# Kernel tuning notes

Hardware: AMD Instinct MI355X
Metric: run time of the kernel (lower is better)

Reference implementation:

```python
import jax, jax.numpy as jnp
import numpy as np

DIM = 768
HEADS = 8
HIDDEN = 3072
B, Hs, Ws = 16, 32, 32
N = Hs * Ws
LN_EPS = 1e-5


def setup_inputs() -> dict:
    key = jax.random.key(0)
    ks = jax.random.split(key, 10)
    s = lambda *sh: 0.02
    return {
        "x": jax.random.normal(ks[0], (B, N, DIM), jnp.float32),
        "Wq": jax.random.normal(ks[1], (DIM, DIM), jnp.float32) * 0.02,
        "temperature": jnp.ones((HEADS, 1, 1), jnp.float32),
        "fc1_w": jax.random.normal(ks[2], (HIDDEN, DIM), jnp.float32) * 0.02,
        "fc1_b": jnp.zeros((HIDDEN,), jnp.float32),
        "dw_w": jax.random.normal(ks[3], (HIDDEN, 1, 3, 3), jnp.float32) * 0.1,
        "dw_b": jnp.zeros((HIDDEN,), jnp.float32),
        "gamma": jnp.ones((HIDDEN,), jnp.float32),
        "fc2_w": jax.random.normal(ks[4], (DIM, HIDDEN), jnp.float32) * 0.02,
        "fc2_b": jnp.zeros((DIM,), jnp.float32),
        "ln_w": jnp.ones((DIM,), jnp.float32),
        "ln_b": jnp.zeros((DIM,), jnp.float32),
        "H": Hs,
        "W": Ws,
    }


def _dwconv(x, w, b, H, W):
    # x: (B, N, hidden) -> depthwise 3x3, pad 1 -> (B, N, hidden)
    Bn, Nn, Ch = x.shape
    img = x.transpose(0, 2, 1).reshape(Bn, Ch, H, W)
    out = jax.lax.conv_general_dilated(
        img, w, window_strides=(1, 1), padding=((1, 1), (1, 1)),
        dimension_numbers=("NCHW", "OIHW", "NCHW"), feature_group_count=Ch)
    out = out + b[None, :, None, None]
    return out.reshape(Bn, Ch, Nn).transpose(0, 2, 1)


def _layernorm(x, w, b):
    mu = x.mean(-1, keepdims=True)
    var = ((x - mu) ** 2).mean(-1, keepdims=True)
    return (x - mu) * jax.lax.rsqrt(var + LN_EPS) * w + b


def reference(x, Wq, temperature, fc1_w, fc1_b, dw_w, dw_b, gamma,
              fc2_w, fc2_b, ln_w, ln_b, H, W):
    # gpd_ratio == active_ratio == 1 -> pre/post scalings cancel
    Bn, Nn, C = x.shape
    h = temperature.shape[0]
    Ch = C // h
    # q/k/v heads: (B, h, N, Ch)
    q = (x @ Wq.T).reshape(Bn, Nn, h, Ch).transpose(0, 2, 1, 3)
    kv = x.reshape(Bn, Nn, h, Ch).transpose(0, 2, 1, 3)
    # channel attention: softmax over N, pool k over Ch, sigmoid gate
    qs = jax.nn.softmax(q, axis=-2).transpose(0, 1, 3, 2)      # (B,h,Ch,N)
    kp = jax.nn.softmax(kv, axis=-2).mean(-1, keepdims=True)    # (B,h,N,1)
    attn = jax.nn.sigmoid(qs @ kp) * temperature                # (B,h,Ch,1)
    # MLP on v (== x after scaling cancels): fc1 -> dwconv residual -> fc2 -> LN
    h1 = x @ fc1_w.T + fc1_b                                    # (B,N,hidden)
    h2 = gamma * _dwconv(h1, dw_w, dw_b, H, W) + h1
    v = _layernorm(h2 @ fc2_w.T + fc2_b, ln_w, ln_b)            # (B,N,C)
    v = v.reshape(Bn, Nn, h, Ch).transpose(0, 2, 1, 3)          # (B,h,N,Ch)
    prod = attn * v.transpose(0, 1, 3, 2)                       # (B,h,Ch,N)
    out = prod.transpose(0, 3, 1, 2).reshape(Bn, Nn, C)
    return out, prod.transpose(0, 1, 3, 2)
```

## Files before the change

### kernel.cpp

```cpp
#include <hip/hip_runtime.h>

#define BATCH 16
#define SEQ   1024
#define DIM   768
#define NHEAD 8
#define CHD   96
#define HID   3072
#define MTOT  (BATCH * SEQ)

using u16 = unsigned short;
typedef __attribute__((ext_vector_type(8))) short bf16x8;
typedef __attribute__((ext_vector_type(4))) float f32x4;

#define AS1 __attribute__((address_space(1)))
#define AS3 __attribute__((address_space(3)))

__device__ inline float bf2f(u16 u) {
    union { unsigned int i; float f; } v; v.i = ((unsigned int)u) << 16; return v.f;
}
__device__ inline u16 f2bf(float f) {
    union { float f; unsigned int i; } v; v.f = f;
    unsigned int r = v.i + 0x7FFFu + ((v.i >> 16) & 1u);
    return (u16)(r >> 16);
}

__device__ inline void gld16(const void* g, void* l) {
    __builtin_amdgcn_global_load_lds((AS1 const void*)g, (AS3 void*)l, 16, 0, 0);
}

template <int BM>
__global__ __launch_bounds__(512) void gemm_p(const u16* __restrict__ A,
                                              const u16* __restrict__ B,
                                              const float* __restrict__ bias,
                                              u16* __restrict__ C1, int N1,
                                              u16* __restrict__ C2,
                                              int M, int N, int K) {
    constexpr int AROUNDS = BM / 128;
    constexpr int ASLOT = BM * 32;
    constexpr int AFOLD = BM / 2;
    constexpr int NFI = BM / 32;
    __shared__ u16 lds[4 * (ASLOT + 8192)];

    const int tid = threadIdx.x;
    const int lane = tid & 63;
    const int wid = tid >> 6;
    const int wm = (wid >> 2) * (BM / 2);
    const int wn = (wid & 3) << 6;

    const int nwg = gridDim.x;
    const int wg = blockIdx.x;
    const int lid = (wg & 7) * (nwg >> 3) + (wg >> 3);
    const int nbx = N >> 8;
    const int mb = lid / nbx, nb = lid - mb * nbx;
    const int m0 = mb * BM, n0 = nb << 8;

    const int sprow = tid >> 3;
    const int s_l = (tid & 7) ^ (sprow & 7);
    const int sgk = (s_l & 3) << 3;
    const u16* pa = A + (size_t)(m0 + (s_l >> 2) * AFOLD + sprow) * K + sgk;
    const u16* pb = B + (size_t)(n0 + (s_l >> 2) * 128 + sprow) * K + sgk;
    const size_t r64K = (size_t)64 * K;

#define STAGE_A(slot, k0) do {                                        \
    gld16(pa + (k0), &lds[(slot) * (ASLOT + 8192) + tid * 8]);        \
    if (AROUNDS == 2)                                                 \
        gld16(pa + (k0) + r64K,                                       \
              &lds[(slot) * (ASLOT + 8192) + 4096 + tid * 8]);        \
} while (0)
#define STAGE_B(slot, k0) do {                                        \
    gld16(pb + (k0), &lds[(slot) * (ASLOT + 8192) + ASLOT + tid * 8]);\
    gld16(pb + (k0) + r64K,                                           \
          &lds[(slot) * (ASLOT + 8192) + ASLOT + 4096 + tid * 8]);    \
} while (0)

    const int lrow = lane & 15;
    const int kg = lane >> 4;
    const int xA = (((wid >> 2) * 4 + kg) ^ (lrow & 7)) << 3;
    const int xB = (((wn >> 7) * 4 + kg) ^ (lrow & 7)) << 3;
    const int bbase = (wn & 64) + lrow;

    f32x4 acc[NFI][4] = {};

    const int NT = K >> 5;
    STAGE_A(0, 0);  STAGE_B(0, 0);
    STAGE_A(1, 32); STAGE_B(1, 32);
    STAGE_A(2, 64); STAGE_B(2, 64);

    for (int t = 0; t < NT; ++t) {
        const int rem = NT - 1 - t;
        if (rem >= 2)      asm volatile("s_waitcnt vmcnt(8)" ::: "memory");
        else if (rem == 1) asm volatile("s_waitcnt vmcnt(4)" ::: "memory");
        else               asm volatile("s_waitcnt vmcnt(0)" ::: "memory");
        __builtin_amdgcn_sched_barrier(0);
        __builtin_amdgcn_s_barrier();

        const u16* Ls = &lds[(t & 3) * (ASLOT + 8192)];
        const int k3 = (t + 3) << 5;

        bf16x8 bfr[4], af[NFI / 2];
#pragma unroll
        for (int j = 0; j < 4; ++j)
            bfr[j] = *(const bf16x8*)&Ls[ASLOT + (bbase + j * 16) * 64 + xB];
#pragma unroll
        for (int i = 0; i < NFI / 2; ++i)
            af[i] = *(const bf16x8*)&Ls[(i * 16 + lrow) * 64 + xA];
        if (rem >= 3) STAGE_A((t + 3) & 3, k3);
        asm volatile("s_waitcnt lgkmcnt(0)" ::: "memory");
        __builtin_amdgcn_sched_barrier(0);
        __builtin_amdgcn_s_setprio(1);
#pragma unroll
        for (int i = 0; i < NFI / 2; ++i)
#pragma unroll
            for (int j = 0; j < 4; ++j)
                acc[i][j] = __builtin_amdgcn_mfma_f32_16x16x32_bf16(af[i], bfr[j], acc[i][j], 0, 0, 0);
        __builtin_amdgcn_s_setprio(0);

        bf16x8 af2[NFI / 2];
#pragma unroll
        for (int i = 0; i < NFI / 2; ++i)
            af2[i] = *(const bf16x8*)&Ls[((i + NFI / 2) * 16 + lrow) * 64 + xA];
        if (rem >= 3) STAGE_B((t + 3) & 3, k3);
        asm volatile("s_waitcnt lgkmcnt(0)" ::: "memory");
        __builtin_amdgcn_sched_barrier(0);
        __builtin_amdgcn_s_setprio(1);
#pragma unroll
        for (int i = 0; i < NFI / 2; ++i)
#pragma unroll
            for (int j = 0; j < 4; ++j)
                acc[i + NFI / 2][j] = __builtin_amdgcn_mfma_f32_16x16x32_bf16(af2[i], bfr[j], acc[i + NFI / 2][j], 0, 0, 0);
        __builtin_amdgcn_s_setprio(0);
    }
#undef STAGE_A
#undef STAGE_B

    __builtin_amdgcn_s_barrier();
    u16* Ct = lds;
    const int crow = (lane >> 4) << 2, ccol = lane & 15;
#pragma unroll
    for (int i = 0; i < NFI; ++i) {
#pragma unroll
        for (int j = 0; j < 4; ++j) {
            const int col = wn + j * 16 + ccol;
            const int gn = n0 + col;
            const float bv = (gn < N1) ? bias[gn] : 0.f;
#pragma unroll
            for (int r = 0; r < 4; ++r) {
                const int row = wm + i * 16 + crow + r;
                const int slot = (col >> 3) ^ (row & 7);
                Ct[row * 256 + slot * 8 + (col & 7)] = f2bf(acc[i][j][r] + bv);
            }
        }
    }
    __builtin_amdgcn_s_barrier();
    const int N2 = N - N1;
#pragma unroll
    for (int k = 0; k < BM / 16; ++k) {
        const int c = tid + (k << 9);
        const int row = c >> 5, s = c & 31;
        bf16x8 v = *(const bf16x8*)&Ct[row * 256 + ((s ^ (row & 7)) << 3)];
        const int gm = m0 + row, gnb = n0 + (s << 3);
        if (gnb < N1)
            *(bf16x8*)&C1[(size_t)gm * N1 + gnb] = v;
        else
            *(bf16x8*)&C2[(size_t)gm * N2 + gnb - N1] = v;
    }
}

__global__ __launch_bounds__(256) void cvt_all(const float* __restrict__ x,
                                               const float* __restrict__ Wq,
                                               const float* __restrict__ w1,
                                               const float* __restrict__ w2,
                                               u16* __restrict__ xb,
                                               u16* __restrict__ Wqb,
                                               u16* __restrict__ w1b,
                                               u16* __restrict__ w2b) {
    const int E0 = MTOT * DIM / 4;
    const int E1 = E0 + DIM * DIM / 4;
    const int E2 = E1 + HID * DIM / 4;
    const int E3 = E2 + DIM * HID / 4;
    int i = blockIdx.x * 256 + threadIdx.x;
    if (i >= E3) return;
    const float* in; u16* out; int k;
    if (i < E0)      { in = x;  out = xb;  k = i; }
    else if (i < E1) { in = Wq; out = Wqb; k = i - E0; }
    else if (i < E2) { in = w1; out = w1b; k = i - E1; }
    else             { in = w2; out = w2b; k = i - E2; }
    float4 v = reinterpret_cast<const float4*>(in)[k];
    ushort4 o;
    o.x = f2bf(v.x); o.y = f2bf(v.y); o.z = f2bf(v.z); o.w = f2bf(v.w);
    reinterpret_cast<ushort4*>(out)[k] = o;
}

__global__ __launch_bounds__(256) void colsm_stats(const u16* __restrict__ X,
                                                   float* __restrict__ Mo,
                                                   float* __restrict__ So) {
    const int tid = threadIdx.x, lane = tid & 63, chunk = tid >> 6;
    const int b = blockIdx.y;
    const int j = blockIdx.x * 64 + lane;
    const u16* p = X + (size_t)b * SEQ * DIM + j;
    float m = -3.0e38f, s = 0.f;
    const int nEnd = (chunk + 1) << 8;
    for (int n = chunk << 8; n < nEnd; ++n) {
        float raw = bf2f(p[(size_t)n * DIM]);
        float nm = fmaxf(m, raw);
        s = s * __expf(m - nm) + __expf(raw - nm);
        m = nm;
    }
    __shared__ float ms[4][64], ss[4][64];
    ms[chunk][lane] = m; ss[chunk][lane] = s;
    __syncthreads();
    if (tid < 64) {
        float M = fmaxf(fmaxf(ms[0][lane], ms[1][lane]), fmaxf(ms[2][lane], ms[3][lane]));
        float S = ss[0][lane] * __expf(ms[0][lane] - M) + ss[1][lane] * __expf(ms[1][lane] - M) +
                  ss[2][lane] * __expf(ms[2][lane] - M) + ss[3][lane] * __expf(ms[3][lane] - M);
        Mo[b * DIM + j] = M;
        So[b * DIM + j] = S;
    }
}

__global__ __launch_bounds__(256) void kp_k(const u16* __restrict__ x,
                                            const float* __restrict__ Mx,
                                            const float* __restrict__ Sx,
                                            float* __restrict__ kp) {
    const int n = blockIdx.x, b = blockIdx.y, tid = threadIdx.x;
    const u16* row = x + ((size_t)b * SEQ + n) * DIM;
    const int h = tid >> 5, c0 = tid & 31;
    const float* Mrow = Mx + b * DIM;
    const float* Srow = Sx + b * DIM;
    float s = 0.f;
#pragma unroll
    for (int q = 0; q < 3; ++q) {
        const int j = h * CHD + c0 + (q << 5);
        s += __expf(bf2f(row[j]) - Mrow[j]) / Srow[j];
    }
#pragma unroll
    for (int o = 16; o; o >>= 1) s += __shfl_down(s, o, 32);
    if (c0 == 0) kp[((size_t)b * NHEAD + h) * SEQ + n] = s * (1.f / (float)CHD);
}

__global__ __launch_bounds__(256) void qattn_k(const u16* __restrict__ Q,
                                               const float* __restrict__ kp,
                                               const float* __restrict__ temp,
                                               float* __restrict__ attnv) {
    const int tid = threadIdx.x, lane = tid & 63, chunk = tid >> 6;
    const int b = blockIdx.y;
    const int j = blockIdx.x * 64 + lane;
    const int h = j / CHD;
    const u16* qp = Q + (size_t)b * SEQ * DIM + j;
    const float* kpp = kp + ((size_t)b * NHEAD + h) * SEQ;
    float m = -3.0e38f, s = 0.f, a = 0.f;
    const int nEnd = (chunk + 1) << 8;
    for (int n = chunk << 8; n < nEnd; ++n) {
        float q = bf2f(qp[(size_t)n * DIM]);
        float nm = fmaxf(m, q);
        float sc = __expf(m - nm), e = __expf(q - nm);
        s = s * sc + e;
        a = a * sc + e * kpp[n];
        m = nm;
    }
    __shared__ float ms[4][64], ss[4][64], as_[4][64];
    ms[chunk][lane] = m; ss[chunk][lane] = s; as_[chunk][lane] = a;
    __syncthreads();
    if (tid < 64) {
        float M = fmaxf(fmaxf(ms[0][lane], ms[1][lane]), fmaxf(ms[2][lane], ms[3][lane]));
        float S = 0.f, A = 0.f;
#pragma unroll
        for (int c = 0; c < 4; ++c) {
            float sc = __expf(ms[c][lane] - M);
            S += ss[c][lane] * sc;
            A += as_[c][lane] * sc;
        }
        float z = A / S;
        attnv[b * DIM + j] = temp[h] / (1.f + __expf(-z));
    }
}

__global__ __launch_bounds__(128) void dwconv_v(const u16* __restrict__ h1,
                                                const float* __restrict__ w,
                                                const float* __restrict__ dwb,
                                                const float* __restrict__ gamma,
                                                u16* __restrict__ h2) {
    const int g = blockIdx.x * 128 + threadIdx.x;
    const int y = blockIdx.y >> 2;
    const int xw0 = (blockIdx.y & 3) << 3;
    const int b = blockIdx.z;
    const int ch0 = g << 3;

    float wreg[8][9], bias2[8];
#pragma unroll
    for (int c = 0; c < 8; ++c) {
        const float gm = gamma[ch0 + c];
#pragma unroll
        for (int k = 0; k < 9; ++k) wreg[c][k] = gm * w[(ch0 + c) * 9 + k];
        wreg[c][4] += 1.0f;
        bias2[c] = gm * dwb[ch0 + c];
    }

    float acc[8][8];
#pragma unroll
    for (int xo = 0; xo < 8; ++xo)
#pragma unroll
        for (int c = 0; c < 8; ++c) acc[xo][c] = bias2[c];

    const u16* base = h1 + (size_t)b * SEQ * HID + ch0;
#pragma unroll
    for (int dy = 0; dy < 3; ++dy) {
        const int yy = y + dy - 1;
        if ((unsigned)yy > 31u) continue;
#pragma unroll
        for (int cr = -1; cr <= 8; ++cr) {
            const int col = xw0 + cr;
            if ((unsigned)col > 31u) continue;
            const uint4 v = *reinterpret_cast<const uint4*>(
                base + (size_t)((yy << 5) + col) * HID);
            float f[8];
            f[0] = bf2f((u16)(v.x & 0xffff)); f[1] = bf2f((u16)(v.x >> 16));
            f[2] = bf2f((u16)(v.y & 0xffff)); f[3] = bf2f((u16)(v.y >> 16));
            f[4] = bf2f((u16)(v.z & 0xffff)); f[5] = bf2f((u16)(v.z >> 16));
            f[6] = bf2f((u16)(v.w & 0xffff)); f[7] = bf2f((u16)(v.w >> 16));
            const int xlo = cr > 0 ? cr - 1 : 0;
            const int xhi = cr < 7 ? cr + 1 : 7;
#pragma unroll
            for (int xo = 0; xo < 8; ++xo) {
                if (xo < xlo || xo > xhi) continue;
                const int dx = cr - xo + 1;
#pragma unroll
                for (int c = 0; c < 8; ++c)
                    acc[xo][c] += f[c] * wreg[c][dy * 3 + dx];
            }
        }
    }

#pragma unroll
    for (int xo = 0; xo < 8; ++xo) {
        const int n = (y << 5) + xw0 + xo;
        uint4 o;
        o.x = (unsigned)f2bf(acc[xo][0]) | ((unsigned)f2bf(acc[xo][1]) << 16);
        o.y = (unsigned)f2bf(acc[xo][2]) | ((unsigned)f2bf(acc[xo][3]) << 16);
        o.z = (unsigned)f2bf(acc[xo][4]) | ((unsigned)f2bf(acc[xo][5]) << 16);
        o.w = (unsigned)f2bf(acc[xo][6]) | ((unsigned)f2bf(acc[xo][7]) << 16);
        *reinterpret_cast<uint4*>(h2 + ((size_t)b * SEQ + n) * HID + ch0) = o;
    }
}

__global__ __launch_bounds__(256) void ln_out_k(const u16* __restrict__ vpre,
                                                const float* __restrict__ lnw,
                                                const float* __restrict__ lnb,
                                                const float* __restrict__ attnv,
                                                float* __restrict__ out,
                                                float* __restrict__ out2) {
    const int n = blockIdx.x, b = blockIdx.y, tid = threadIdx.x;
    __shared__ float red[4];
    const u16* row = vpre + ((size_t)b * SEQ + n) * DIM;
    float v[3];
    float s = 0.f;
#pragma unroll
    for (int q = 0; q < 3; ++q) { v[q] = bf2f(row[tid + (q << 8)]); s += v[q]; }
#pragma unroll
    for (int o = 32; o; o >>= 1) s += __shfl_down(s, o, 64);
    if ((tid & 63) == 0) red[tid >> 6] = s;
    __syncthreads();
    const float mu = (red[0] + red[1] + red[2] + red[3]) * (1.f / (float)DIM);
    __syncthreads();
    float vs = 0.f;
#pragma unroll
    for (int q = 0; q < 3; ++q) { float d = v[q] - mu; vs += d * d; }
#pragma unroll
    for (int o = 32; o; o >>= 1) vs += __shfl_down(vs, o, 64);
    if ((tid & 63) == 0) red[tid >> 6] = vs;
    __syncthreads();
    const float rstd = rsqrtf((red[0] + red[1] + red[2] + red[3]) * (1.f / (float)DIM) + 1e-5f);
    const float* at = attnv + b * DIM;
    float* orow = out + ((size_t)b * SEQ + n) * DIM;
#pragma unroll
    for (int q = 0; q < 3; ++q) {
        int j = tid + (q << 8);
        float o = (v[q] - mu) * rstd * lnw[j] + lnb[j];
        o *= at[j];
        orow[j] = o;
        int h = j / CHD, c = j - h * CHD;
        out2[(((size_t)b * NHEAD + h) * SEQ + n) * CHD + c] = o;
    }
}

extern "C" void kernel_launch(void* const* d_in, const int* in_sizes, int n_in,
                              void* d_out, int out_size, void* d_ws, size_t ws_size,
                              hipStream_t stream) {
    const float* x     = (const float*)d_in[0];
    const float* Wq    = (const float*)d_in[1];
    const float* temp  = (const float*)d_in[2];
    const float* fc1w  = (const float*)d_in[3];
    const float* fc1b  = (const float*)d_in[4];
    const float* dww   = (const float*)d_in[5];
    const float* dwb   = (const float*)d_in[6];
    const float* gamma = (const float*)d_in[7];
    const float* fc2w  = (const float*)d_in[8];
    const float* fc2b  = (const float*)d_in[9];
    const float* lnw   = (const float*)d_in[10];
    const float* lnb   = (const float*)d_in[11];

    float* out  = (float*)d_out;
    float* out2 = out + (size_t)BATCH * SEQ * DIM;

    char* ws = (char*)d_ws;
    u16* xb     = (u16*)ws;
    u16* h1     = (u16*)(ws + 25165824);
    u16* Bbig   = (u16*)(ws + 125829120);
    u16* Wqb    = Bbig + (size_t)HID * DIM;
    u16* fc2wb  = (u16*)(ws + 131727360);
    float* Mx   = (float*)(ws + 136445952);
    float* Sx   = Mx + BATCH * DIM;
    float* kp   = Sx + BATCH * DIM;
    float* attnv = kp + BATCH * NHEAD * SEQ;
    u16* vpreb  = xb;

    u16* Qb = (u16*)d_out;
    u16* h2 = (u16*)d_out;

    {
        const int tot4 = (MTOT * DIM + DIM * DIM + HID * DIM + DIM * HID) / 4;
        cvt_all<<<(tot4 + 255) / 256, 256, 0, stream>>>(
            x, Wq, fc1w, fc2w, xb, Wqb, Bbig, fc2wb);
    }

    gemm_p<256><<<(MTOT / 256) * (3840 / 256), 512, 0, stream>>>(
        xb, Bbig, fc1b, h1, HID, Qb, MTOT, HID + DIM, DIM);

    colsm_stats<<<dim3(DIM / 64, BATCH), 256, 0, stream>>>(xb, Mx, Sx);
    kp_k<<<dim3(SEQ, BATCH), 256, 0, stream>>>(xb, Mx, Sx, kp);
    qattn_k<<<dim3(DIM / 64, BATCH), 256, 0, stream>>>(Qb, kp, temp, attnv);

    dwconv_v<<<dim3(3, 128, BATCH), 128, 0, stream>>>(h1, dww, dwb, gamma, h2);
    gemm_p<256><<<(MTOT / 256) * (DIM / 256), 512, 0, stream>>>(
        h2, fc2wb, fc2b, vpreb, DIM, (u16*)nullptr, MTOT, DIM, HID);
    ln_out_k<<<dim3(SEQ, BATCH), 256, 0, stream>>>(vpreb, lnw, lnb, attnv, out, out2);
}
```

Measured before the change: 377.8 us.

## Load B fragments directly from global memory, staging only A through LDS

The GEMM no longer stages the B tile through LDS. Each wave now reads its B fragments straight from global memory into registers every k-step, while A keeps the 4-slot global_load_lds ring. This shrinks LDS use and is meant to raise occupancy and cut LDS traffic, at the cost of uncoalesced direct global reads of B and some exposed latency. To fit the smaller LDS, the epilogue writes the C tile in two halves, and the vmcnt wait counts are retuned for the new number of outstanding loads.

```diff
diff --git a/kernel.cpp b/kernel.cpp
--- a/kernel.cpp
+++ b/kernel.cpp
@@ -39,12 +39,12 @@
     constexpr int ASLOT = BM * 32;
     constexpr int AFOLD = BM / 2;
     constexpr int NFI = BM / 32;
-    __shared__ u16 lds[4 * (ASLOT + 8192)];
+    __shared__ u16 lds[4 * ASLOT];
 
     const int tid = threadIdx.x;
     const int lane = tid & 63;
     const int wid = tid >> 6;
-    const int wm = (wid >> 2) * (BM / 2);
+    const int wm = (wid >> 2) * AFOLD;
     const int wn = (wid & 3) << 6;
 
     const int nwg = gridDim.x;
@@ -58,49 +58,52 @@
     const int s_l = (tid & 7) ^ (sprow & 7);
     const int sgk = (s_l & 3) << 3;
     const u16* pa = A + (size_t)(m0 + (s_l >> 2) * AFOLD + sprow) * K + sgk;
-    const u16* pb = B + (size_t)(n0 + (s_l >> 2) * 128 + sprow) * K + sgk;
     const size_t r64K = (size_t)64 * K;
 
 #define STAGE_A(slot, k0) do {                                        \
-    gld16(pa + (k0), &lds[(slot) * (ASLOT + 8192) + tid * 8]);        \
+    gld16(pa + (k0), &lds[(slot) * ASLOT + tid * 8]);                 \
     if (AROUNDS == 2)                                                 \
-        gld16(pa + (k0) + r64K,                                       \
-              &lds[(slot) * (ASLOT + 8192) + 4096 + tid * 8]);        \
-} while (0)
-#define STAGE_B(slot, k0) do {                                        \
-    gld16(pb + (k0), &lds[(slot) * (ASLOT + 8192) + ASLOT + tid * 8]);\
-    gld16(pb + (k0) + r64K,                                           \
-          &lds[(slot) * (ASLOT + 8192) + ASLOT + 4096 + tid * 8]);    \
+        gld16(pa + (k0) + r64K, &lds[(slot) * ASLOT + 4096 + tid * 8]);\
 } while (0)
 
     const int lrow = lane & 15;
     const int kg = lane >> 4;
     const int xA = (((wid >> 2) * 4 + kg) ^ (lrow & 7)) << 3;
-    const int xB = (((wn >> 7) * 4 + kg) ^ (lrow & 7)) << 3;
-    const int bbase = (wn & 64) + lrow;
+    const u16* Bp = B + (size_t)(n0 + wn + lrow) * K + (kg << 3);
 
     f32x4 acc[NFI][4] = {};
 
     const int NT = K >> 5;
-    STAGE_A(0, 0);  STAGE_B(0, 0);
-    STAGE_A(1, 32); STAGE_B(1, 32);
-    STAGE_A(2, 64); STAGE_B(2, 64);
+    STAGE_A(0, 0);
+    STAGE_A(1, 32);
+    STAGE_A(2, 64);
 
     for (int t = 0; t < NT; ++t) {
         const int rem = NT - 1 - t;
-        if (rem >= 2)      asm volatile("s_waitcnt vmcnt(8)" ::: "memory");
-        else if (rem == 1) asm volatile("s_waitcnt vmcnt(4)" ::: "memory");
-        else               asm volatile("s_waitcnt vmcnt(0)" ::: "memory");
+        if (t >= 2) {
+            if constexpr (AROUNDS == 2) asm volatile("s_waitcnt vmcnt(12)" ::: "memory");
+            else                        asm volatile("s_waitcnt vmcnt(10)" ::: "memory");
+        } else if (t == 1) {
+            if constexpr (AROUNDS == 2) asm volatile("s_waitcnt vmcnt(8)" ::: "memory");
+            else                        asm volatile("s_waitcnt vmcnt(6)" ::: "memory");
+        } else {
+            if constexpr (AROUNDS == 2) asm volatile("s_waitcnt vmcnt(4)" ::: "memory");
+            else                        asm volatile("s_waitcnt vmcnt(2)" ::: "memory");
+        }
         __builtin_amdgcn_sched_barrier(0);
         __builtin_amdgcn_s_barrier();
-
-        const u16* Ls = &lds[(t & 3) * (ASLOT + 8192)];
+        __builtin_amdgcn_sched_barrier(0);
+
+        bf16x8 bfr[4];
+#pragma unroll
+        for (int j = 0; j < 4; ++j)
+            bfr[j] = *(const bf16x8*)(Bp + (size_t)(j * 16) * K + (t << 5));
+        __builtin_amdgcn_sched_barrier(0);
+
+        const u16* Ls = &lds[(t & 3) * ASLOT];
         const int k3 = (t + 3) << 5;
 
-        bf16x8 bfr[4], af[NFI / 2];
-#pragma unroll
-        for (int j = 0; j < 4; ++j)
-            bfr[j] = *(const bf16x8*)&Ls[ASLOT + (bbase + j * 16) * 64 + xB];
+        bf16x8 af[NFI / 2];
 #pragma unroll
         for (int i = 0; i < NFI / 2; ++i)
             af[i] = *(const bf16x8*)&Ls[(i * 16 + lrow) * 64 + xA];
@@ -119,7 +122,6 @@
 #pragma unroll
         for (int i = 0; i < NFI / 2; ++i)
             af2[i] = *(const bf16x8*)&Ls[((i + NFI / 2) * 16 + lrow) * 64 + xA];
-        if (rem >= 3) STAGE_B((t + 3) & 3, k3);
         asm volatile("s_waitcnt lgkmcnt(0)" ::: "memory");
         __builtin_amdgcn_sched_barrier(0);
         __builtin_amdgcn_s_setprio(1);
@@ -131,38 +133,40 @@
         __builtin_amdgcn_s_setprio(0);
     }
 #undef STAGE_A
-#undef STAGE_B
-
-    __builtin_amdgcn_s_barrier();
-    u16* Ct = lds;
+
+    constexpr int RP = BM / 2;
     const int crow = (lane >> 4) << 2, ccol = lane & 15;
-#pragma unroll
-    for (int i = 0; i < NFI; ++i) {
-#pragma unroll
-        for (int j = 0; j < 4; ++j) {
-            const int col = wn + j * 16 + ccol;
-            const int gn = n0 + col;
-            const float bv = (gn < N1) ? bias[gn] : 0.f;
-#pragma unroll
-            for (int r = 0; r < 4; ++r) {
-                const int row = wm + i * 16 + crow + r;
-                const int slot = (col >> 3) ^ (row & 7);
-                Ct[row * 256 + slot * 8 + (col & 7)] = f2bf(acc[i][j][r] + bv);
+    const int N2 = N - N1;
+#pragma unroll
+    for (int p = 0; p < 2; ++p) {
+        __builtin_amdgcn_s_barrier();
+        if ((wid >> 2) == p) {
+#pragma unroll
+            for (int i = 0; i < NFI; ++i) {
+#pragma unroll
+                for (int j = 0; j < 4; ++j) {
+                    const int col = wn + j * 16 + ccol;
+                    const int gn = n0 + col;
+                    const float bv = (gn < N1 && bias) ? bias[gn] : 0.f;
+#pragma unroll
+                    for (int r = 0; r < 4; ++r) {
+                        const int lr = i * 16 + crow + r;
+                        lds[lr * 256 + (((col >> 3) ^ (lr & 7)) << 3) + (col & 7)] =
+                            f2bf(acc[i][j][r] + bv);
+                    }
+                }
             }
         }
-    }
-    __builtin_amdgcn_s_barrier();
-    const int N2 = N - N1;
-#pragma unroll
-    for (int k = 0; k < BM / 16; ++k) {
-        const int c = tid + (k << 9);
-        const int row = c >> 5, s = c & 31;
-        bf16x8 v = *(const bf16x8*)&Ct[row * 256 + ((s ^ (row & 7)) << 3)];
-        const int gm = m0 + row, gnb = n0 + (s << 3);
-        if (gnb < N1)
-            *(bf16x8*)&C1[(size_t)gm * N1 + gnb] = v;
-        else
-            *(bf16x8*)&C2[(size_t)gm * N2 + gnb - N1] = v;
+        __builtin_amdgcn_s_barrier();
+#pragma unroll
+        for (int k = 0; k < RP / 16; ++k) {
+            const int c = tid + (k << 9);
+            const int r = c >> 5, s = c & 31;
+            bf16x8 v = *(const bf16x8*)&lds[r * 256 + ((s ^ (r & 7)) << 3)];
+            const int gm = m0 + p * RP + r, gnb = n0 + (s << 3);
+            if (gnb < N1) *(bf16x8*)&C1[(size_t)gm * N1 + gnb] = v;
+            else          *(bf16x8*)&C2[(size_t)gm * N2 + gnb - N1] = v;
+        }
     }
 }
 
```

Result: slower. 525.5 us (+39.1%).

## Restructure bf16 GEMM to BK=64 double-buffered quadrant pipeline with interleaved staging

Applied to the files above, without the earlier changes.

Rewrites the GEMM main loop to use K-tiles of 64 with two LDS buffers instead of four 32-wide buffers. Each iteration is split into four MFMA quadrant phases, and the global-to-LDS staging of the next tile is spread across them in quarter pieces so loads overlap compute. This aims to halve the number of loop iterations and barrier waits per K while keeping the same 256x256 block tile. In exchange it adds more barriers inside each iteration and keeps only one tile of prefetch depth, and the bias load is now guarded against a null pointer.

```diff
diff --git a/kernel.cpp b/kernel.cpp
--- a/kernel.cpp
+++ b/kernel.cpp
@@ -28,23 +28,17 @@
     __builtin_amdgcn_global_load_lds((AS1 const void*)g, (AS3 void*)l, 16, 0, 0);
 }
 
-template <int BM>
 __global__ __launch_bounds__(512) void gemm_p(const u16* __restrict__ A,
                                               const u16* __restrict__ B,
                                               const float* __restrict__ bias,
                                               u16* __restrict__ C1, int N1,
                                               u16* __restrict__ C2,
                                               int M, int N, int K) {
-    constexpr int AROUNDS = BM / 128;
-    constexpr int ASLOT = BM * 32;
-    constexpr int AFOLD = BM / 2;
-    constexpr int NFI = BM / 32;
-    __shared__ u16 lds[4 * (ASLOT + 8192)];
-
+    __shared__ u16 lds[65536];
     const int tid = threadIdx.x;
     const int lane = tid & 63;
     const int wid = tid >> 6;
-    const int wm = (wid >> 2) * (BM / 2);
+    const int wm = (wid >> 2) << 7;
     const int wn = (wid & 3) << 6;
 
     const int nwg = gridDim.x;
@@ -52,97 +46,144 @@
     const int lid = (wg & 7) * (nwg >> 3) + (wg >> 3);
     const int nbx = N >> 8;
     const int mb = lid / nbx, nb = lid - mb * nbx;
-    const int m0 = mb * BM, n0 = nb << 8;
-
-    const int sprow = tid >> 3;
-    const int s_l = (tid & 7) ^ (sprow & 7);
-    const int sgk = (s_l & 3) << 3;
-    const u16* pa = A + (size_t)(m0 + (s_l >> 2) * AFOLD + sprow) * K + sgk;
-    const u16* pb = B + (size_t)(n0 + (s_l >> 2) * 128 + sprow) * K + sgk;
+    const int m0 = mb << 8, n0 = nb << 8;
+
+    const int srow = tid >> 3;
+    const int sl = (tid & 7) ^ (srow & 7);
+    const u16* pa = A + (size_t)(m0 + srow) * K + sl * 8;
+    const u16* pb = B + (size_t)(n0 + srow) * K + sl * 8;
     const size_t r64K = (size_t)64 * K;
-
-#define STAGE_A(slot, k0) do {                                        \
-    gld16(pa + (k0), &lds[(slot) * (ASLOT + 8192) + tid * 8]);        \
-    if (AROUNDS == 2)                                                 \
-        gld16(pa + (k0) + r64K,                                       \
-              &lds[(slot) * (ASLOT + 8192) + 4096 + tid * 8]);        \
-} while (0)
-#define STAGE_B(slot, k0) do {                                        \
-    gld16(pb + (k0), &lds[(slot) * (ASLOT + 8192) + ASLOT + tid * 8]);\
-    gld16(pb + (k0) + r64K,                                           \
-          &lds[(slot) * (ASLOT + 8192) + ASLOT + 4096 + tid * 8]);    \
+    const size_t r128K = r64K * 2;
+
+#define STAGE(op, half, buf, kt) do {                                        \
+    const u16* s_ = ((op) ? pb : pa) + (half) * r128K + (size_t)(kt) * 64;   \
+    u16* d_ = &lds[(buf) * 32768 + (op) * 16384 + (half) * 8192 + tid * 8];  \
+    gld16(s_, d_);                                                           \
+    gld16(s_ + r64K, d_ + 4096);                                             \
 } while (0)
 
     const int lrow = lane & 15;
     const int kg = lane >> 4;
-    const int xA = (((wid >> 2) * 4 + kg) ^ (lrow & 7)) << 3;
-    const int xB = (((wn >> 7) * 4 + kg) ^ (lrow & 7)) << 3;
-    const int bbase = (wn & 64) + lrow;
-
-    f32x4 acc[NFI][4] = {};
-
-    const int NT = K >> 5;
-    STAGE_A(0, 0);  STAGE_B(0, 0);
-    STAGE_A(1, 32); STAGE_B(1, 32);
-    STAGE_A(2, 64); STAGE_B(2, 64);
+    const int sw = lrow & 7;
+    const int cA0 = ((kg ^ sw) << 3);
+    const int cA1 = (((4 + kg) ^ sw) << 3);
+    const int ahalf = wid >> 2;
+    const int bhalf = (wid & 3) >> 1;
+    const int wnr = (wid & 1) << 6;
+
+    f32x4 acc[8][4] = {};
+
+    const int NT = K >> 6;
+    STAGE(0, 0, 0, 0); STAGE(0, 1, 0, 0);
+    STAGE(1, 0, 0, 0); STAGE(1, 1, 0, 0);
+    STAGE(0, 0, 1, 1);
+    asm volatile("s_waitcnt vmcnt(2)" ::: "memory");
+    __builtin_amdgcn_sched_barrier(0);
+    __builtin_amdgcn_s_barrier();
 
     for (int t = 0; t < NT; ++t) {
-        const int rem = NT - 1 - t;
-        if (rem >= 2)      asm volatile("s_waitcnt vmcnt(8)" ::: "memory");
-        else if (rem == 1) asm volatile("s_waitcnt vmcnt(4)" ::: "memory");
-        else               asm volatile("s_waitcnt vmcnt(0)" ::: "memory");
-        __builtin_amdgcn_sched_barrier(0);
-        __builtin_amdgcn_s_barrier();
-
-        const u16* Ls = &lds[(t & 3) * (ASLOT + 8192)];
-        const int k3 = (t + 3) << 5;
-
-        bf16x8 bfr[4], af[NFI / 2];
-#pragma unroll
-        for (int j = 0; j < 4; ++j)
-            bfr[j] = *(const bf16x8*)&Ls[ASLOT + (bbase + j * 16) * 64 + xB];
-#pragma unroll
-        for (int i = 0; i < NFI / 2; ++i)
-            af[i] = *(const bf16x8*)&Ls[(i * 16 + lrow) * 64 + xA];
-        if (rem >= 3) STAGE_A((t + 3) & 3, k3);
+        const int buf = t & 1, nbuf = buf ^ 1;
+        const u16* LA = &lds[buf * 32768 + ahalf * 8192];
+        const u16* LB = &lds[buf * 32768 + 16384 + bhalf * 8192];
+        const bool pre1 = (t + 1 < NT);
+
+        bf16x8 a03[4][2], b01[2][2];
+#pragma unroll
+        for (int mi = 0; mi < 4; ++mi) {
+            a03[mi][0] = *(const bf16x8*)&LA[(mi * 16 + lrow) * 64 + cA0];
+            a03[mi][1] = *(const bf16x8*)&LA[(mi * 16 + lrow) * 64 + cA1];
+        }
+#pragma unroll
+        for (int nj = 0; nj < 2; ++nj) {
+            b01[nj][0] = *(const bf16x8*)&LB[(wnr + nj * 16 + lrow) * 64 + cA0];
+            b01[nj][1] = *(const bf16x8*)&LB[(wnr + nj * 16 + lrow) * 64 + cA1];
+        }
+        if (pre1) STAGE(0, 1, nbuf, t + 1);
+        __builtin_amdgcn_s_barrier();
         asm volatile("s_waitcnt lgkmcnt(0)" ::: "memory");
         __builtin_amdgcn_sched_barrier(0);
         __builtin_amdgcn_s_setprio(1);
 #pragma unroll
-        for (int i = 0; i < NFI / 2; ++i)
-#pragma unroll
-            for (int j = 0; j < 4; ++j)
-                acc[i][j] = __builtin_amdgcn_mfma_f32_16x16x32_bf16(af[i], bfr[j], acc[i][j], 0, 0, 0);
+        for (int mi = 0; mi < 4; ++mi)
+#pragma unroll
+            for (int nj = 0; nj < 2; ++nj) {
+                acc[mi][nj] = __builtin_amdgcn_mfma_f32_16x16x32_bf16(a03[mi][0], b01[nj][0], acc[mi][nj], 0, 0, 0);
+                acc[mi][nj] = __builtin_amdgcn_mfma_f32_16x16x32_bf16(a03[mi][1], b01[nj][1], acc[mi][nj], 0, 0, 0);
+            }
         __builtin_amdgcn_s_setprio(0);
-
-        bf16x8 af2[NFI / 2];
-#pragma unroll
-        for (int i = 0; i < NFI / 2; ++i)
-            af2[i] = *(const bf16x8*)&Ls[((i + NFI / 2) * 16 + lrow) * 64 + xA];
-        if (rem >= 3) STAGE_B((t + 3) & 3, k3);
+        __builtin_amdgcn_s_barrier();
+
+        bf16x8 b23[2][2];
+#pragma unroll
+        for (int nj = 0; nj < 2; ++nj) {
+            b23[nj][0] = *(const bf16x8*)&LB[(wnr + (nj + 2) * 16 + lrow) * 64 + cA0];
+            b23[nj][1] = *(const bf16x8*)&LB[(wnr + (nj + 2) * 16 + lrow) * 64 + cA1];
+        }
+        if (pre1) STAGE(1, 0, nbuf, t + 1);
+        __builtin_amdgcn_s_barrier();
         asm volatile("s_waitcnt lgkmcnt(0)" ::: "memory");
         __builtin_amdgcn_sched_barrier(0);
         __builtin_amdgcn_s_setprio(1);
 #pragma unroll
-        for (int i = 0; i < NFI / 2; ++i)
-#pragma unroll
-            for (int j = 0; j < 4; ++j)
-                acc[i + NFI / 2][j] = __builtin_amdgcn_mfma_f32_16x16x32_bf16(af2[i], bfr[j], acc[i + NFI / 2][j], 0, 0, 0);
+        for (int mi = 0; mi < 4; ++mi)
+#pragma unroll
+            for (int nj = 0; nj < 2; ++nj) {
+                acc[mi][nj + 2] = __builtin_amdgcn_mfma_f32_16x16x32_bf16(a03[mi][0], b23[nj][0], acc[mi][nj + 2], 0, 0, 0);
+                acc[mi][nj + 2] = __builtin_amdgcn_mfma_f32_16x16x32_bf16(a03[mi][1], b23[nj][1], acc[mi][nj + 2], 0, 0, 0);
+            }
         __builtin_amdgcn_s_setprio(0);
-    }
-#undef STAGE_A
-#undef STAGE_B
+        __builtin_amdgcn_s_barrier();
+
+        bf16x8 a47[4][2];
+#pragma unroll
+        for (int mi = 0; mi < 4; ++mi) {
+            a47[mi][0] = *(const bf16x8*)&LA[((mi + 4) * 16 + lrow) * 64 + cA0];
+            a47[mi][1] = *(const bf16x8*)&LA[((mi + 4) * 16 + lrow) * 64 + cA1];
+        }
+        if (pre1) STAGE(1, 1, nbuf, t + 1);
+        __builtin_amdgcn_s_barrier();
+        asm volatile("s_waitcnt lgkmcnt(0)" ::: "memory");
+        __builtin_amdgcn_sched_barrier(0);
+        __builtin_amdgcn_s_setprio(1);
+#pragma unroll
+        for (int mi = 0; mi < 4; ++mi)
+#pragma unroll
+            for (int nj = 0; nj < 2; ++nj) {
+                acc[mi + 4][nj] = __builtin_amdgcn_mfma_f32_16x16x32_bf16(a47[mi][0], b01[nj][0], acc[mi + 4][nj], 0, 0, 0);
+                acc[mi + 4][nj] = __builtin_amdgcn_mfma_f32_16x16x32_bf16(a47[mi][1], b01[nj][1], acc[mi + 4][nj], 0, 0, 0);
+            }
+        __builtin_amdgcn_s_setprio(0);
+        __builtin_amdgcn_s_barrier();
+
+        if (t + 2 < NT) STAGE(0, 0, buf, t + 2);
+        __builtin_amdgcn_s_setprio(1);
+#pragma unroll
+        for (int mi = 0; mi < 4; ++mi)
+#pragma unroll
+            for (int nj = 0; nj < 2; ++nj) {
+                acc[mi + 4][nj + 2] = __builtin_amdgcn_mfma_f32_16x16x32_bf16(a47[mi][0], b23[nj][0], acc[mi + 4][nj + 2], 0, 0, 0);
+                acc[mi + 4][nj + 2] = __builtin_amdgcn_mfma_f32_16x16x32_bf16(a47[mi][1], b23[nj][1], acc[mi + 4][nj + 2], 0, 0, 0);
+            }
+        __builtin_amdgcn_s_setprio(0);
+        if (t < NT - 1) {
+            if (t + 2 < NT) asm volatile("s_waitcnt vmcnt(2)" ::: "memory");
+            else            asm volatile("s_waitcnt vmcnt(0)" ::: "memory");
+            __builtin_amdgcn_sched_barrier(0);
+            __builtin_amdgcn_s_barrier();
+        }
+    }
+#undef STAGE
 
     __builtin_amdgcn_s_barrier();
     u16* Ct = lds;
     const int crow = (lane >> 4) << 2, ccol = lane & 15;
 #pragma unroll
-    for (int i = 0; i < NFI; ++i) {
+    for (int i = 0; i < 8; ++i) {
 #pragma unroll
         for (int j = 0; j < 4; ++j) {
             const int col = wn + j * 16 + ccol;
             const int gn = n0 + col;
-            const float bv = (gn < N1) ? bias[gn] : 0.f;
+            const float bv = (gn < N1 && bias) ? bias[gn] : 0.f;
 #pragma unroll
             for (int r = 0; r < 4; ++r) {
                 const int row = wm + i * 16 + crow + r;
@@ -154,7 +195,7 @@
     __builtin_amdgcn_s_barrier();
     const int N2 = N - N1;
 #pragma unroll
-    for (int k = 0; k < BM / 16; ++k) {
+    for (int k = 0; k < 16; ++k) {
         const int c = tid + (k << 9);
         const int row = c >> 5, s = c & 31;
         bf16x8 v = *(const bf16x8*)&Ct[row * 256 + ((s ^ (row & 7)) << 3)];
@@ -423,7 +464,7 @@
             x, Wq, fc1w, fc2w, xb, Wqb, Bbig, fc2wb);
     }
 
-    gemm_p<256><<<(MTOT / 256) * (3840 / 256), 512, 0, stream>>>(
+    gemm_p<<<(MTOT / 256) * (3840 / 256), 512, 0, stream>>>(
         xb, Bbig, fc1b, h1, HID, Qb, MTOT, HID + DIM, DIM);
 
     colsm_stats<<<dim3(DIM / 64, BATCH), 256, 0, stream>>>(xb, Mx, Sx);
@@ -431,7 +472,7 @@
     qattn_k<<<dim3(DIM / 64, BATCH), 256, 0, stream>>>(Qb, kp, temp, attnv);
 
     dwconv_v<<<dim3(3, 128, BATCH), 128, 0, stream>>>(h1, dww, dwb, gamma, h2);
-    gemm_p<256><<<(MTOT / 256) * (DIM / 256), 512, 0, stream>>>(
+    gemm_p<<<(MTOT / 256) * (DIM / 256), 512, 0, stream>>>(
         h2, fc2wb, fc2b, vpreb, DIM, (u16*)nullptr, MTOT, DIM, HID);
     ln_out_k<<<dim3(SEQ, BATCH), 256, 0, stream>>>(vpreb, lnw, lnb, attnv, out, out2);
 }
```

Measured after the change: 385.2 us. No clear change (+2.0%).
